# Kernel optimization log

Measured on AMD Instinct MI355X. Metric: run time of the kernel, lower is better.

The kernel has to match this reference:

```python
import jax, jax.numpy as jnp
import numpy as np

EPS = 1e-8          # torch nn.CosineSimilarity default eps
DIST_THR = 31.5     # 0.7 * 45 (module default)


def setup_inputs() -> dict:
    key = jax.random.key(0)
    k1, k2, k3, k4, k5 = jax.random.split(key, 5)
    B, C, H, W = 8, 256, 48, 48
    y = jax.random.normal(k1, (B, C, H, W), dtype=jnp.float32)
    yp = jax.random.normal(k2, (B, C, H, W), dtype=jnp.float32)
    z = jax.random.normal(k3, (B, C, H, W), dtype=jnp.float32)
    zp = jax.random.normal(k4, (B, C, H, W), dtype=jnp.float32)
    # distances in [0, 63): threshold 31.5 selects ~half of the pairs
    distances = jax.random.uniform(k5, (H, W, H, W), dtype=jnp.float32) * 63.0
    return {"y": y, "yp": yp, "z": z, "zp": zp, "distances": distances}


def _pairwise_cosine(a, b):
    # a, b: [B, C, N]; returns [B, N, N] cosine similarity over channel dim,
    # equivalent to CosineSimilarity(dim=1)(a[..., None], b[..., None, :])
    # but without materializing the [B, C, N, N] broadcast intermediate.
    dots = jnp.einsum('bcn,bcm->bnm', a, b)                       # [B,N,N]
    na = jnp.maximum(jnp.linalg.norm(a, axis=1), EPS)             # [B,N]
    nb = jnp.maximum(jnp.linalg.norm(b, axis=1), EPS)             # [B,N]
    return dots / (na[:, :, None] * nb[:, None, :])


def reference(y, yp, z, zp, distances):
    B, C = y.shape[0], y.shape[1]
    yf = y.reshape(B, C, -1)    # [B,C,N]
    ypf = yp.reshape(B, C, -1)
    zf = z.reshape(B, C, -1)
    zpf = zp.reshape(B, C, -1)

    cos_y_zp = _pairwise_cosine(yf, zpf)   # [B,N,N]
    cos_yp_z = _pairwise_cosine(zf, ypf)   # [B,N,N]

    H1, W1, H2, W2 = distances.shape
    mask = (distances.reshape(H1 * W1, H2 * W2) < DIST_THR)       # [N,N]

    # masked_select with mask broadcast over batch, then mean:
    # mean over B * count(mask) selected elements of -(cos1 + cos2)
    s = jnp.sum(jnp.where(mask[None, :, :], cos_y_zp + cos_yp_z, 0.0))
    cnt = jnp.sum(mask).astype(s.dtype) * B
    return -s / cnt
```

## Files before the change

kernel.cpp:

```cpp
#include <hip/hip_runtime.h>
#include <stdint.h>

#define GLOBAL_AS __attribute__((address_space(1)))
#define LDS_AS __attribute__((address_space(3)))

typedef _Float16 half_t;
typedef _Float16 f16x8 __attribute__((ext_vector_type(8)));
typedef float f32x4 __attribute__((ext_vector_type(4)));

static constexpr int BATCH = 8;
static constexpr int CH = 256;
static constexpr int N = 2304;
static constexpr int KTOT = 4096;
static constexpr int MW = 72;
static constexpr int MWORDS = 165888;
static constexpr int LROW = 258;
static constexpr float EPS = 1e-8f;
static constexpr float THR = 31.5f;
static constexpr int NBLK = 243;


__global__ __launch_bounds__(256) void prep_kernel(
    const float* __restrict__ y, const float* __restrict__ yp,
    const float* __restrict__ z, const float* __restrict__ zp,
    const float* __restrict__ dist,
    half_t* __restrict__ At, half_t* __restrict__ Bt,
    uint32_t* __restrict__ maskw, unsigned int* __restrict__ c_part) {
  const int t = threadIdx.x;
  const int bz = blockIdx.z;

  if (bz >= 4) {
    const int blk = ((bz - 4) * 8 + blockIdx.y) * 36 + blockIdx.x;
    const int w = blk * 256 + t;
    int c = 0;
    if (w < MWORDS) {
      const float4* p = (const float4*)(dist + (size_t)w * 32);
      uint32_t bits = 0;
#pragma unroll
      for (int q = 0; q < 8; ++q) {
        float4 v = p[q];
        bits |= (v.x < THR ? 1u : 0u) << (q * 4);
        bits |= (v.y < THR ? 1u : 0u) << (q * 4 + 1);
        bits |= (v.z < THR ? 1u : 0u) << (q * 4 + 2);
        bits |= (v.w < THR ? 1u : 0u) << (q * 4 + 3);
      }
      maskw[w] = bits;
      c = __popc(bits);
    }
#pragma unroll
    for (int off = 32; off; off >>= 1) c += __shfl_down(c, off, 64);
    __shared__ int mred[4];
    if ((t & 63) == 0) mred[t >> 6] = c;
    __syncthreads();
    if (t == 0)
      c_part[blk] = (unsigned int)(mred[0] + mred[1] + mred[2] + mred[3]);
    return;
  }

  const int b = blockIdx.y;
  const int n0 = blockIdx.x * 64;
  const float* src; half_t* dst; int kh;
  switch (bz) {
    case 0:  src = y;  dst = At; kh = 0;    break;
    case 1:  src = z;  dst = At; kh = 2048; break;
    case 2:  src = zp; dst = Bt; kh = 0;    break;
    default: src = yp; dst = Bt; kh = 2048; break;
  }
  const int kbase = kh + b * 256;
  const int col4 = (t & 15) * 4;
  const int cb = t >> 4;

  const float* base = src + (size_t)(b * CH + cb * 16) * N + n0 + col4;
  float4 v[16];
#pragma unroll
  for (int i = 0; i < 16; ++i) v[i] = *(const float4*)(base + (size_t)i * N);

  float ss[4] = {0.f, 0.f, 0.f, 0.f};
#pragma unroll
  for (int i = 0; i < 16; ++i) {
    ss[0] = fmaf(v[i].x, v[i].x, ss[0]);
    ss[1] = fmaf(v[i].y, v[i].y, ss[1]);
    ss[2] = fmaf(v[i].z, v[i].z, ss[2]);
    ss[3] = fmaf(v[i].w, v[i].w, ss[3]);
  }
  __shared__ float partial[16][65];
  __shared__ float sc[64];
  __shared__ half_t tile[64 * LROW];
#pragma unroll
  for (int j = 0; j < 4; ++j) partial[cb][col4 + j] = ss[j];
  __syncthreads();
  if (t < 64) {
    float s = 0.f;
#pragma unroll
    for (int k = 0; k < 16; ++k) s += partial[k][t];
    sc[t] = 1.0f / fmaxf(sqrtf(s), EPS);
  }
  __syncthreads();

#pragma unroll
  for (int j = 0; j < 4; ++j) {
    const float scj = sc[col4 + j];
    union { half_t h[16]; f16x8 v2[2]; } u;
#pragma unroll
    for (int i = 0; i < 16; ++i)
      u.h[i] = (half_t)(((const float*)&v[i])[j] * scj);
    f16x8* q = (f16x8*)(tile + (col4 + j) * LROW + cb * 16);
    q[0] = u.v2[0];
    q[1] = u.v2[1];
  }
  __syncthreads();

  {
    const int r = t >> 4, c = t & 15;
#pragma unroll
    for (int p = 0; p < 4; ++p) {
      const int row = p * 16 + r;
      half_t* gout = dst + (size_t)(n0 + row) * KTOT + kbase;
      const half_t* lrow = tile + row * LROW;
#pragma unroll
      for (int inst = 0; inst < 2; ++inst) {
        const int off = c * 8 + inst * 128;
        *(f16x8*)(gout + off) = *(const f16x8*)(lrow + off);
      }
    }
  }
}

__global__ __launch_bounds__(512, 2) void gemm_kernel(
    const half_t* __restrict__ At, const half_t* __restrict__ Bt,
    const uint32_t* __restrict__ maskw, float* __restrict__ s_part) {
  __shared__ __align__(16) half_t As[2 * 16384];
  __shared__ __align__(16) half_t Bs[2 * 16384];
  __shared__ float red[8];

  const int t = threadIdx.x;
  const int lane = t & 63;
  const int w8 = t >> 6;

  const int orig = blockIdx.x;
  const int xcd = orig & 7;
  const int wid = (xcd < 3 ? xcd * 31 : 93 + (xcd - 3) * 30) + (orig >> 3);
  const int zt = wid / 81;
  const int t81 = wid % 81;
  const int n0 = (t81 / 9) * 256;
  const int m0 = (t81 % 9) * 256;
  const int k0 = zt * 1408;
  const int NI = (zt == 2) ? 10 : 11;

  const int srow = t >> 3;
  const int schunk8 = ((t & 7) ^ (srow & 7)) * 8;
  const half_t* gA = At + (size_t)(n0 + srow) * KTOT + k0 + schunk8;
  const half_t* gB = Bt + (size_t)(m0 + srow) * KTOT + k0 + schunk8;
  const int ldsw = w8 * 512;

  auto SA = [&](int tl, int u, int buf) {
    __builtin_amdgcn_global_load_lds(
        (const GLOBAL_AS void*)(gA + (size_t)(u * 64) * KTOT + tl * 64),
        (LDS_AS void*)(As + buf * 16384 + u * 4096 + ldsw), 16, 0, 0);
  };
  auto SB = [&](int tl, int u, int buf) {
    __builtin_amdgcn_global_load_lds(
        (const GLOBAL_AS void*)(gB + (size_t)(u * 64) * KTOT + tl * 64),
        (LDS_AS void*)(Bs + buf * 16384 + u * 4096 + ldsw), 16, 0, 0);
  };

  const int fr = lane & 15;
  const int cl = lane >> 4;
  const int e = lane & 7;
  const int ksw0 = ((((cl ^ e) & 3)) | (e & 4)) * 8;
  const int ksw1 = ksw0 ^ 32;
  const int wA = w8 >> 2;
  const int wB = w8 & 3;
  const int aoff = (wA * 128 + fr) * 64;
  const int boff = (wB * 64 + fr) * 64;

  f32x4 acc[8][4] = {};
  f16x8 af[4], bf[4];

#define RD_A(BUF, QA, KSW)                                                     \
  _Pragma("unroll") for (int i = 0; i < 4; ++i)                                \
      af[i] = *(const f16x8*)(As + (BUF) * 16384 + aoff + (QA) * 4096 +        \
                              i * 1024 + (KSW));
#define RD_B(BUF, KSW)                                                         \
  _Pragma("unroll") for (int j = 0; j < 4; ++j)                                \
      bf[j] = *(const f16x8*)(Bs + (BUF) * 16384 + boff + j * 1024 + (KSW));
#define MM(QA)                                                                 \
  __builtin_amdgcn_s_setprio(1);                                               \
  _Pragma("unroll") for (int i = 0; i < 4; ++i)                                \
    _Pragma("unroll") for (int j = 0; j < 4; ++j)                              \
      acc[(QA) * 4 + i][j] = __builtin_amdgcn_mfma_f32_16x16x32_f16(           \
          af[i], bf[j], acc[(QA) * 4 + i][j], 0, 0, 0);                        \
  __builtin_amdgcn_s_setprio(0);
#define BARMID                                                                 \
  __builtin_amdgcn_s_barrier();                                                \
  asm volatile("s_waitcnt lgkmcnt(0)" ::: "memory");
#define BAREND __builtin_amdgcn_s_barrier();

#define ITER(SN)                                                               \
  {                                                                            \
    const int u = 2 * j + 1, t2 = 2 * j + 2, t3 = 2 * j + 3;                   \
                                                             \
    RD_A(0, 0, ksw0); RD_B(0, ksw0);                                           \
    SA(u, 1, 1); SA(u, 3, 1);                                                  \
    BARMID; MM(0); BAREND;                                                     \
                                                             \
    RD_A(0, 1, ksw0);                                                          \
    SB(u, 0, 1); SB(u, 1, 1);                                                  \
    BARMID; MM(1); BAREND;                                                     \
                                                             \
    RD_A(0, 0, ksw1); RD_B(0, ksw1);                                           \
    SB(u, 2, 1); SB(u, 3, 1);                                                  \
    BARMID; MM(0); BAREND;                                                     \
                                               \
    RD_A(0, 1, ksw1);                                                          \
    if (SN) {                                                                  \
      SA(t2, 0, 0); SA(t2, 2, 0);                                              \
      asm volatile("s_waitcnt vmcnt(2)" ::: "memory");                         \
    } else {                                                                   \
      asm volatile("s_waitcnt vmcnt(0)" ::: "memory");                         \
    }                                                                          \
    BARMID; MM(1); BAREND;                                                     \
                                                        \
    RD_A(1, 0, ksw0); RD_B(1, ksw0);                                           \
    if (SN) { SA(t2, 1, 0); SA(t2, 3, 0); }                                    \
    BARMID; MM(0); BAREND;                                                     \
                                                                       \
    RD_A(1, 1, ksw0);                                                          \
    if (SN) { SB(t2, 0, 0); SB(t2, 1, 0); }                                    \
    BARMID; MM(1); BAREND;                                                     \
                                                                       \
    RD_A(1, 0, ksw1); RD_B(1, ksw1);                                           \
    if (SN) { SB(t2, 2, 0); SB(t2, 3, 0); }                                    \
    BARMID; MM(0); BAREND;                                                     \
                                                        \
    RD_A(1, 1, ksw1);                                                          \
    if (SN) {                                                                  \
      SA(t3, 0, 1); SA(t3, 2, 1);                                              \
      asm volatile("s_waitcnt vmcnt(2)" ::: "memory");                         \
    }                                                                          \
    BARMID; MM(1); BAREND;                                                     \
  }

  SA(0, 0, 0); SA(0, 1, 0); SA(0, 2, 0); SA(0, 3, 0);
  SB(0, 0, 0); SB(0, 1, 0); SB(0, 2, 0); SB(0, 3, 0);
  SA(1, 0, 1); SA(1, 2, 1);
  asm volatile("s_waitcnt vmcnt(2)" ::: "memory");
  __builtin_amdgcn_s_barrier();

  int j = 0;
  for (; j < NI - 1; ++j) ITER(true);
  ITER(false);
#undef ITER
#undef RD_A
#undef RD_B
#undef MM
#undef BARMID
#undef BAREND

  float local = 0.f;
  const int mw0 = (m0 + wB * 64) >> 5;
#pragma unroll
  for (int i = 0; i < 8; ++i) {
    const int ng = n0 + wA * 128 + i * 16 + cl * 4;
#pragma unroll
    for (int r = 0; r < 4; ++r) {
      const uint2 wv = *(const uint2*)(maskw + (size_t)(ng + r) * MW + mw0);
#pragma unroll
      for (int j2 = 0; j2 < 4; ++j2) {
        const uint32_t ww = (j2 & 2) ? wv.y : wv.x;
        if ((ww >> (fr + ((j2 & 1) << 4))) & 1u) local += acc[i][j2][r];
      }
    }
  }
#pragma unroll
  for (int off = 32; off; off >>= 1) local += __shfl_down(local, off, 64);
  if (lane == 0) red[w8] = local;
  __syncthreads();
  if (t == 0) {
    float s = 0.f;
#pragma unroll
    for (int k = 0; k < 8; ++k) s += red[k];
    s_part[orig] = s;
  }
}

__global__ void finalize_kernel(const float* __restrict__ s_part,
                                const unsigned int* __restrict__ c_part,
                                float* __restrict__ out) {
  const int t = threadIdx.x;
  float local = 0.f;
  for (int i = t; i < NBLK; i += 256) local += s_part[i];
  unsigned int clocal = 0;
  for (int i = t; i < 864; i += 256) clocal += c_part[i];
#pragma unroll
  for (int off = 32; off; off >>= 1) {
    local += __shfl_down(local, off, 64);
    clocal += __shfl_down(clocal, off, 64);
  }
  __shared__ float red[4];
  __shared__ unsigned int credu[4];
  if ((t & 63) == 0) { red[t >> 6] = local; credu[t >> 6] = clocal; }
  __syncthreads();
  if (t == 0) {
    const float s = red[0] + red[1] + red[2] + red[3];
    const float cnt = (float)(credu[0] + credu[1] + credu[2] + credu[3]);
    out[0] = -s / (cnt * (float)BATCH);
  }
}

extern "C" void kernel_launch(void* const* d_in, const int* in_sizes, int n_in,
                              void* d_out, int out_size, void* d_ws, size_t ws_size,
                              hipStream_t stream) {
  const float* y    = (const float*)d_in[0];
  const float* yp   = (const float*)d_in[1];
  const float* z    = (const float*)d_in[2];
  const float* zp   = (const float*)d_in[3];
  const float* dist = (const float*)d_in[4];
  float* out = (float*)d_out;

  char* ws = (char*)d_ws;
  float* s_part = (float*)ws;
  unsigned int* c_part = (unsigned int*)(ws + 8192);
  half_t* At = (half_t*)(ws + 16384);
  half_t* Bt = (half_t*)(ws + 16384 + 18874368);
  uint32_t* maskw = (uint32_t*)(ws + 16384 + 2 * 18874368);

  prep_kernel<<<dim3(36, 8, 7), 256, 0, stream>>>(y, yp, z, zp, dist, At, Bt, maskw, c_part);
  gemm_kernel<<<dim3(NBLK), 512, 0, stream>>>(At, Bt, maskw, s_part);
  finalize_kernel<<<1, 256, 0, stream>>>(s_part, c_part, out);
}
```

Before: 175.9 us.

## Double-buffer MFMA fragment registers to overlap LDS reads with matrix math

Splits the A/B fragment registers into two ping-pong sets so the LDS reads for the next sub-step are issued after the barrier while the MFMAs for the current sub-step run on the other set. This is meant to hide LDS read latency behind MFMA work instead of serialising read, wait, then compute. A prologue preloads the first fragments and the last sub-step prefetches for the next iteration. In exchange, more VGPRs are live, which can lower occupancy or cause spills, and the correctness of the barrier and wait ordering now depends on LDS buffer reuse timing.

```diff
diff --git a/kernel.cpp b/kernel.cpp
--- a/kernel.cpp
+++ b/kernel.cpp
@@ -175,21 +175,21 @@
   const int boff = (wB * 64 + fr) * 64;
 
   f32x4 acc[8][4] = {};
-  f16x8 af[4], bf[4];
-
-#define RD_A(BUF, QA, KSW)                                                     \
+  f16x8 afX[4], afY[4], bfX[4], bfY[4];
+
+#define RD_A(DST, BUF, QA, KSW)                                                \
   _Pragma("unroll") for (int i = 0; i < 4; ++i)                                \
-      af[i] = *(const f16x8*)(As + (BUF) * 16384 + aoff + (QA) * 4096 +        \
-                              i * 1024 + (KSW));
-#define RD_B(BUF, KSW)                                                         \
-  _Pragma("unroll") for (int j = 0; j < 4; ++j)                                \
-      bf[j] = *(const f16x8*)(Bs + (BUF) * 16384 + boff + j * 1024 + (KSW));
-#define MM(QA)                                                                 \
+      DST[i] = *(const f16x8*)(As + (BUF) * 16384 + aoff + (QA) * 4096 +       \
+                               i * 1024 + (KSW));
+#define RD_B(DST, BUF, KSW)                                                    \
+  _Pragma("unroll") for (int j_ = 0; j_ < 4; ++j_)                             \
+      DST[j_] = *(const f16x8*)(Bs + (BUF) * 16384 + boff + j_ * 1024 + (KSW));
+#define MM(QA, AF, BF)                                                         \
   __builtin_amdgcn_s_setprio(1);                                               \
-  _Pragma("unroll") for (int i = 0; i < 4; ++i)                                \
-    _Pragma("unroll") for (int j = 0; j < 4; ++j)                              \
-      acc[(QA) * 4 + i][j] = __builtin_amdgcn_mfma_f32_16x16x32_f16(           \
-          af[i], bf[j], acc[(QA) * 4 + i][j], 0, 0, 0);                        \
+  _Pragma("unroll") for (int i_ = 0; i_ < 4; ++i_)                             \
+    _Pragma("unroll") for (int j_ = 0; j_ < 4; ++j_)                           \
+      acc[(QA) * 4 + i_][j_] = __builtin_amdgcn_mfma_f32_16x16x32_f16(         \
+          AF[i_], BF[j_], acc[(QA) * 4 + i_][j_], 0, 0, 0);                    \
   __builtin_amdgcn_s_setprio(0);
 #define BARMID                                                                 \
   __builtin_amdgcn_s_barrier();                                                \
@@ -199,46 +199,54 @@
 #define ITER(SN)                                                               \
   {                                                                            \
     const int u = 2 * j + 1, t2 = 2 * j + 2, t3 = 2 * j + 3;                   \
-                                                             \
-    RD_A(0, 0, ksw0); RD_B(0, ksw0);                                           \
+                    \
     SA(u, 1, 1); SA(u, 3, 1);                                                  \
-    BARMID; MM(0); BAREND;                                                     \
-                                                             \
-    RD_A(0, 1, ksw0);                                                          \
+    BARMID;                                                                    \
+    RD_A(afY, 0, 1, ksw0);                                                     \
+    MM(0, afX, bfX); BAREND;                                                   \
+                    \
     SB(u, 0, 1); SB(u, 1, 1);                                                  \
-    BARMID; MM(1); BAREND;                                                     \
-                                                             \
-    RD_A(0, 0, ksw1); RD_B(0, ksw1);                                           \
+    BARMID;                                                                    \
+    RD_A(afX, 0, 0, ksw1); RD_B(bfY, 0, ksw1);                                 \
+    MM(1, afY, bfX); BAREND;                                                   \
+                    \
     SB(u, 2, 1); SB(u, 3, 1);                                                  \
-    BARMID; MM(0); BAREND;                                                     \
-                                               \
-    RD_A(0, 1, ksw1);                                                          \
+    BARMID;                                                                    \
+    RD_A(afY, 0, 1, ksw1);                                                     \
+    MM(0, afX, bfY); BAREND;                                                   \
+       \
     if (SN) {                                                                  \
       SA(t2, 0, 0); SA(t2, 2, 0);                                              \
       asm volatile("s_waitcnt vmcnt(2)" ::: "memory");                         \
     } else {                                                                   \
       asm volatile("s_waitcnt vmcnt(0)" ::: "memory");                         \
     }                                                                          \
-    BARMID; MM(1); BAREND;                                                     \
-                                                        \
-    RD_A(1, 0, ksw0); RD_B(1, ksw0);                                           \
+    BARMID;                                                                    \
+    RD_A(afX, 1, 0, ksw0); RD_B(bfX, 1, ksw0);                                 \
+    MM(1, afY, bfY); BAREND;                                                   \
+                    \
     if (SN) { SA(t2, 1, 0); SA(t2, 3, 0); }                                    \
-    BARMID; MM(0); BAREND;                                                     \
-                                                                       \
-    RD_A(1, 1, ksw0);                                                          \
+    BARMID;                                                                    \
+    RD_A(afY, 1, 1, ksw0);                                                     \
+    MM(0, afX, bfX); BAREND;                                                   \
+                    \
     if (SN) { SB(t2, 0, 0); SB(t2, 1, 0); }                                    \
-    BARMID; MM(1); BAREND;                                                     \
-                                                                       \
-    RD_A(1, 0, ksw1); RD_B(1, ksw1);                                           \
+    BARMID;                                                                    \
+    RD_A(afX, 1, 0, ksw1); RD_B(bfY, 1, ksw1);                                 \
+    MM(1, afY, bfX); BAREND;                                                   \
+                    \
     if (SN) { SB(t2, 2, 0); SB(t2, 3, 0); }                                    \
-    BARMID; MM(0); BAREND;                                                     \
-                                                        \
-    RD_A(1, 1, ksw1);                                                          \
+    BARMID;                                                                    \
+    RD_A(afY, 1, 1, ksw1);                                                     \
+    MM(0, afX, bfY); BAREND;                                                   \
+            \
     if (SN) {                                                                  \
       SA(t3, 0, 1); SA(t3, 2, 1);                                              \
       asm volatile("s_waitcnt vmcnt(2)" ::: "memory");                         \
     }                                                                          \
-    BARMID; MM(1); BAREND;                                                     \
+    BARMID;                                                                    \
+    if (SN) { RD_A(afX, 0, 0, ksw0); RD_B(bfX, 0, ksw0); }                     \
+    MM(1, afY, bfY); BAREND;                                                   \
   }
 
   SA(0, 0, 0); SA(0, 1, 0); SA(0, 2, 0); SA(0, 3, 0);
@@ -246,6 +254,8 @@
   SA(1, 0, 1); SA(1, 2, 1);
   asm volatile("s_waitcnt vmcnt(2)" ::: "memory");
   __builtin_amdgcn_s_barrier();
+  RD_A(afX, 0, 0, ksw0);
+  RD_B(bfX, 0, ksw0);
 
   int j = 0;
   for (; j < NI - 1; ++j) ITER(true);
```

Result: slower. 182.5 us (+3.7%).

## Shrink GEMM tiles to 128x128 with 256 threads and simpler double-buffer loop

Applied to the files above, without the earlier changes.

Changes the masked GEMM from 256x256 tiles with 512-thread blocks and 3-way split-K (243 blocks) to 128x128 tiles with 256-thread blocks and 3-way split-K (972 blocks). The finely interleaved 8-phase prefetch schedule is replaced with a plain double-buffered loop that issues the whole next k-tile, then waits with vmcnt(0) before the second half. The aim is better load balance and occupancy across CUs with smaller LDS use. In exchange each block reuses less data per tile, so global and LDS traffic rises, and the new schedule overlaps loads with compute less.

```diff
diff --git a/kernel.cpp b/kernel.cpp
--- a/kernel.cpp
+++ b/kernel.cpp
@@ -17,7 +17,7 @@
 static constexpr int LROW = 258;
 static constexpr float EPS = 1e-8f;
 static constexpr float THR = 31.5f;
-static constexpr int NBLK = 243;
+static constexpr int NBLK = 972;
 
 
 __global__ __launch_bounds__(256) void prep_kernel(
@@ -126,42 +126,42 @@
   }
 }
 
-__global__ __launch_bounds__(512, 2) void gemm_kernel(
+__global__ __launch_bounds__(256, 2) void gemm_kernel(
     const half_t* __restrict__ At, const half_t* __restrict__ Bt,
     const uint32_t* __restrict__ maskw, float* __restrict__ s_part) {
-  __shared__ __align__(16) half_t As[2 * 16384];
-  __shared__ __align__(16) half_t Bs[2 * 16384];
-  __shared__ float red[8];
+  __shared__ __align__(16) half_t As[2 * 8192];
+  __shared__ __align__(16) half_t Bs[2 * 8192];
+  __shared__ float red[4];
 
   const int t = threadIdx.x;
   const int lane = t & 63;
-  const int w8 = t >> 6;
+  const int w4 = t >> 6;
 
   const int orig = blockIdx.x;
   const int xcd = orig & 7;
-  const int wid = (xcd < 3 ? xcd * 31 : 93 + (xcd - 3) * 30) + (orig >> 3);
-  const int zt = wid / 81;
-  const int t81 = wid % 81;
-  const int n0 = (t81 / 9) * 256;
-  const int m0 = (t81 % 9) * 256;
-  const int k0 = zt * 1408;
-  const int NI = (zt == 2) ? 10 : 11;
+  const int wid = (xcd < 4 ? xcd * 122 : 488 + (xcd - 4) * 121) + (orig >> 3);
+  const int zt = wid / 324;
+  const int t324 = wid % 324;
+  const int n0 = (t324 / 18) * 128;
+  const int m0 = (t324 % 18) * 128;
+  const int k0 = zt ? (1408 + (zt - 1) * 1344) : 0;
+  const int NT = zt ? 21 : 22;
 
   const int srow = t >> 3;
   const int schunk8 = ((t & 7) ^ (srow & 7)) * 8;
   const half_t* gA = At + (size_t)(n0 + srow) * KTOT + k0 + schunk8;
   const half_t* gB = Bt + (size_t)(m0 + srow) * KTOT + k0 + schunk8;
-  const int ldsw = w8 * 512;
+  const int ldsw = w4 * 512;
 
   auto SA = [&](int tl, int u, int buf) {
     __builtin_amdgcn_global_load_lds(
-        (const GLOBAL_AS void*)(gA + (size_t)(u * 64) * KTOT + tl * 64),
-        (LDS_AS void*)(As + buf * 16384 + u * 4096 + ldsw), 16, 0, 0);
+        (const GLOBAL_AS void*)(gA + (size_t)(u * 32) * KTOT + tl * 64),
+        (LDS_AS void*)(As + buf * 8192 + u * 2048 + ldsw), 16, 0, 0);
   };
   auto SB = [&](int tl, int u, int buf) {
     __builtin_amdgcn_global_load_lds(
-        (const GLOBAL_AS void*)(gB + (size_t)(u * 64) * KTOT + tl * 64),
-        (LDS_AS void*)(Bs + buf * 16384 + u * 4096 + ldsw), 16, 0, 0);
+        (const GLOBAL_AS void*)(gB + (size_t)(u * 32) * KTOT + tl * 64),
+        (LDS_AS void*)(Bs + buf * 8192 + u * 2048 + ldsw), 16, 0, 0);
   };
 
   const int fr = lane & 15;
@@ -169,88 +169,52 @@
   const int e = lane & 7;
   const int ksw0 = ((((cl ^ e) & 3)) | (e & 4)) * 8;
   const int ksw1 = ksw0 ^ 32;
-  const int wA = w8 >> 2;
-  const int wB = w8 & 3;
-  const int aoff = (wA * 128 + fr) * 64;
+  const int wA = w4 >> 1;
+  const int wB = w4 & 1;
+  const int aoff = (wA * 64 + fr) * 64;
   const int boff = (wB * 64 + fr) * 64;
 
-  f32x4 acc[8][4] = {};
+  f32x4 acc[4][4] = {};
   f16x8 af[4], bf[4];
 
-#define RD_A(BUF, QA, KSW)                                                     \
+#define RD_A(BUF, KSW)                                                         \
   _Pragma("unroll") for (int i = 0; i < 4; ++i)                                \
-      af[i] = *(const f16x8*)(As + (BUF) * 16384 + aoff + (QA) * 4096 +        \
-                              i * 1024 + (KSW));
+      af[i] = *(const f16x8*)(As + (BUF) * 8192 + aoff + i * 1024 + (KSW));
 #define RD_B(BUF, KSW)                                                         \
-  _Pragma("unroll") for (int j = 0; j < 4; ++j)                                \
-      bf[j] = *(const f16x8*)(Bs + (BUF) * 16384 + boff + j * 1024 + (KSW));
-#define MM(QA)                                                                 \
+  _Pragma("unroll") for (int j_ = 0; j_ < 4; ++j_)                             \
+      bf[j_] = *(const f16x8*)(Bs + (BUF) * 8192 + boff + j_ * 1024 + (KSW));
+#define MM                                                                     \
   __builtin_amdgcn_s_setprio(1);                                               \
-  _Pragma("unroll") for (int i = 0; i < 4; ++i)                                \
-    _Pragma("unroll") for (int j = 0; j < 4; ++j)                              \
-      acc[(QA) * 4 + i][j] = __builtin_amdgcn_mfma_f32_16x16x32_f16(           \
-          af[i], bf[j], acc[(QA) * 4 + i][j], 0, 0, 0);                        \
+  _Pragma("unroll") for (int i_ = 0; i_ < 4; ++i_)                             \
+    _Pragma("unroll") for (int j_ = 0; j_ < 4; ++j_)                           \
+      acc[i_][j_] = __builtin_amdgcn_mfma_f32_16x16x32_f16(                    \
+          af[i_], bf[j_], acc[i_][j_], 0, 0, 0);                               \
   __builtin_amdgcn_s_setprio(0);
 #define BARMID                                                                 \
   __builtin_amdgcn_s_barrier();                                                \
   asm volatile("s_waitcnt lgkmcnt(0)" ::: "memory");
 #define BAREND __builtin_amdgcn_s_barrier();
 
-#define ITER(SN)                                                               \
-  {                                                                            \
-    const int u = 2 * j + 1, t2 = 2 * j + 2, t3 = 2 * j + 3;                   \
-                                                             \
-    RD_A(0, 0, ksw0); RD_B(0, ksw0);                                           \
-    SA(u, 1, 1); SA(u, 3, 1);                                                  \
-    BARMID; MM(0); BAREND;                                                     \
-                                                             \
-    RD_A(0, 1, ksw0);                                                          \
-    SB(u, 0, 1); SB(u, 1, 1);                                                  \
-    BARMID; MM(1); BAREND;                                                     \
-                                                             \
-    RD_A(0, 0, ksw1); RD_B(0, ksw1);                                           \
-    SB(u, 2, 1); SB(u, 3, 1);                                                  \
-    BARMID; MM(0); BAREND;                                                     \
-                                               \
-    RD_A(0, 1, ksw1);                                                          \
-    if (SN) {                                                                  \
-      SA(t2, 0, 0); SA(t2, 2, 0);                                              \
-      asm volatile("s_waitcnt vmcnt(2)" ::: "memory");                         \
-    } else {                                                                   \
-      asm volatile("s_waitcnt vmcnt(0)" ::: "memory");                         \
-    }                                                                          \
-    BARMID; MM(1); BAREND;                                                     \
-                                                        \
-    RD_A(1, 0, ksw0); RD_B(1, ksw0);                                           \
-    if (SN) { SA(t2, 1, 0); SA(t2, 3, 0); }                                    \
-    BARMID; MM(0); BAREND;                                                     \
-                                                                       \
-    RD_A(1, 1, ksw0);                                                          \
-    if (SN) { SB(t2, 0, 0); SB(t2, 1, 0); }                                    \
-    BARMID; MM(1); BAREND;                                                     \
-                                                                       \
-    RD_A(1, 0, ksw1); RD_B(1, ksw1);                                           \
-    if (SN) { SB(t2, 2, 0); SB(t2, 3, 0); }                                    \
-    BARMID; MM(0); BAREND;                                                     \
-                                                        \
-    RD_A(1, 1, ksw1);                                                          \
-    if (SN) {                                                                  \
-      SA(t3, 0, 1); SA(t3, 2, 1);                                              \
-      asm volatile("s_waitcnt vmcnt(2)" ::: "memory");                         \
-    }                                                                          \
-    BARMID; MM(1); BAREND;                                                     \
-  }
-
   SA(0, 0, 0); SA(0, 1, 0); SA(0, 2, 0); SA(0, 3, 0);
   SB(0, 0, 0); SB(0, 1, 0); SB(0, 2, 0); SB(0, 3, 0);
-  SA(1, 0, 1); SA(1, 2, 1);
-  asm volatile("s_waitcnt vmcnt(2)" ::: "memory");
+  asm volatile("s_waitcnt vmcnt(0)" ::: "memory");
   __builtin_amdgcn_s_barrier();
 
-  int j = 0;
-  for (; j < NI - 1; ++j) ITER(true);
-  ITER(false);
-#undef ITER
+  for (int j = 0; j < NT; ++j) {
+    const int buf = j & 1;
+    const bool sn = (j + 1 < NT);
+    RD_A(buf, ksw0); RD_B(buf, ksw0);
+    if (sn) {
+      SA(j + 1, 0, buf ^ 1); SA(j + 1, 1, buf ^ 1);
+      SA(j + 1, 2, buf ^ 1); SA(j + 1, 3, buf ^ 1);
+      SB(j + 1, 0, buf ^ 1); SB(j + 1, 1, buf ^ 1);
+      SB(j + 1, 2, buf ^ 1); SB(j + 1, 3, buf ^ 1);
+    }
+    BARMID; MM; BAREND;
+    RD_A(buf, ksw1); RD_B(buf, ksw1);
+    asm volatile("s_waitcnt vmcnt(0)" ::: "memory");
+    BARMID; MM; BAREND;
+  }
 #undef RD_A
 #undef RD_B
 #undef MM
@@ -260,8 +224,8 @@
   float local = 0.f;
   const int mw0 = (m0 + wB * 64) >> 5;
 #pragma unroll
-  for (int i = 0; i < 8; ++i) {
-    const int ng = n0 + wA * 128 + i * 16 + cl * 4;
+  for (int i = 0; i < 4; ++i) {
+    const int ng = n0 + wA * 64 + i * 16 + cl * 4;
 #pragma unroll
     for (int r = 0; r < 4; ++r) {
       const uint2 wv = *(const uint2*)(maskw + (size_t)(ng + r) * MW + mw0);
@@ -274,14 +238,9 @@
   }
 #pragma unroll
   for (int off = 32; off; off >>= 1) local += __shfl_down(local, off, 64);
-  if (lane == 0) red[w8] = local;
-  __syncthreads();
-  if (t == 0) {
-    float s = 0.f;
-#pragma unroll
-    for (int k = 0; k < 8; ++k) s += red[k];
-    s_part[orig] = s;
-  }
+  if (lane == 0) red[w4] = local;
+  __syncthreads();
+  if (t == 0) s_part[orig] = red[0] + red[1] + red[2] + red[3];
 }
 
 __global__ void finalize_kernel(const float* __restrict__ s_part,
@@ -326,6 +285,6 @@
   uint32_t* maskw = (uint32_t*)(ws + 16384 + 2 * 18874368);
 
   prep_kernel<<<dim3(36, 8, 7), 256, 0, stream>>>(y, yp, z, zp, dist, At, Bt, maskw, c_part);
-  gemm_kernel<<<dim3(NBLK), 512, 0, stream>>>(At, Bt, maskw, s_part);
+  gemm_kernel<<<dim3(NBLK), 256, 0, stream>>>(At, Bt, maskw, s_part);
   finalize_kernel<<<1, 256, 0, stream>>>(s_part, c_part, out);
 }
```

Measured after the change: 176.9 us. Within noise of the previous version (+0.5%).
